# Performance work log

Measured on AMD Instinct MI355X. Metric: run time of the kernel, lower is better.

The kernel has to match this reference:

```python
import jax, jax.numpy as jnp
import numpy as np


def setup_inputs() -> dict:
    key = jax.random.key(0)
    k1, k2, k3, k4 = jax.random.split(key, 4)
    B, C = 32768, 10
    x = jax.random.normal(k1, (B, 1, 28, 28), dtype=jnp.float32)
    linear_weight = jax.random.normal(k2, (4 * 14 * 14 + 1 + 2, C), dtype=jnp.float32)
    linear_bias = jax.random.normal(k3, (C,), dtype=jnp.float32)
    sampler_weights = jax.random.normal(k4, (4,), dtype=jnp.float32)
    return {"x": x, "linear_weight": linear_weight, "linear_bias": linear_bias,
            "sampler_weights": sampler_weights}


def reference(x, linear_weight, linear_bias, sampler_weights):
    # Closed-form simulation of the 4-qubit circuits:
    # RY(t)|0> -> <Z>=cos(t); after CX(0,1): <Z1> = cos(t0)*cos(t1); CX(2,3) likewise.
    B = x.shape[0]
    # Extract non-overlapping 2x2 patches in row-major order -> (B, 196, 4)
    p = x[:, 0].reshape(B, 14, 2, 14, 2).transpose(0, 1, 3, 2, 4).reshape(B, 196, 4)
    c = jnp.cos(p)
    # quanvolution_circuit per patch: [cos a, cos a cos b, cos c, cos c cos d]
    feats = jnp.stack([c[..., 0], c[..., 0] * c[..., 1],
                       c[..., 2], c[..., 2] * c[..., 3]], axis=-1)  # (B,196,4)
    qfeat = feats.reshape(B, 784)
    # fully_connected_circuit on qfeat[:, :4]: mean of the four post-CX <Z>
    cf = jnp.cos(qfeat[:, :4])
    qfc = (cf[:, 0] + cf[:, 0] * cf[:, 1] + cf[:, 2] + cf[:, 2] * cf[:, 3]) / 4.0  # (B,)
    # sampler_circuit: sequential RY angles add on wires 0 and 1
    t0 = qfeat[:, 0] + sampler_weights[0] + sampler_weights[2]
    t1 = qfeat[:, 1] + sampler_weights[1] + sampler_weights[3]
    z0 = jnp.cos(t0)
    z1 = z0 * jnp.cos(t1)
    sampler = jax.nn.softmax(jnp.stack([z0, z1], axis=-1), axis=-1)  # (B,2)
    combined = jnp.concatenate([qfeat, qfc[:, None], sampler], axis=-1)  # (B,787)
    logits = combined @ linear_weight + linear_bias
    return jax.nn.log_softmax(logits, axis=-1)
```

## Files before the change

### kernel.cpp

```cpp
#include <hip/hip_runtime.h>


#define ROWF 128

__global__ __launch_bounds__(256, 2)
void qml_fused(const float* __restrict__ x,
               const float* __restrict__ wm,
               const float* __restrict__ bias,
               const float* __restrict__ sw,
               float* __restrict__ out,
               int B)
{
    __shared__ float lds[2][64 * ROWF];

    const int t = threadIdx.x;
    const int lane = t & 63;
    const int wv = __builtin_amdgcn_readfirstlane((int)(t >> 6));
    const int g = blockIdx.x;

    int sample = g * 64 + lane;
    const bool s_ok = (sample < B);
    if (sample >= B) sample = B - 1;

    const float* xb[7];
    int d0[7], d1[7];
#pragma unroll
    for (int k = 0; k < 7; ++k) {
        const int f = k * 256 + t;
        const int s = f / 28;
        const int c = f - 28 * s;
        int sg = g * 64 + s; if (sg >= B) sg = B - 1;
        xb[k] = x + (size_t)sg * 784 + 4 * c;
        const int m2 = (s & 15) << 1;
        d0[k] = s * ROWF + ((4 * c) ^ m2);
        d1[k] = s * ROWF + ((4 * c + 2) ^ m2);
    }

    const int i_loc = wv >> 1;
    const int jbase = 7 * (wv & 1);
    const int o_top = i_loc * 56 + 2 * jbase;
    const int m2c = (lane & 15) << 1;

    float acc[10];
#pragma unroll
    for (int c = 0; c < 10; ++c) acc[c] = 0.0f;
    float q0 = 0.f, q1 = 0.f, q2 = 0.f, q3 = 0.f;

    float4 pre[7];

#pragma unroll
    for (int k = 0; k < 7; ++k) pre[k] = *(const float4*)(xb[k]);
#pragma unroll
    for (int k = 0; k < 7; ++k) {
        *(float2*)(&lds[0][0] + d0[k]) = make_float2(pre[k].x, pre[k].y);
        *(float2*)(&lds[0][0] + d1[k]) = make_float2(pre[k].z, pre[k].w);
    }
    __syncthreads();

#pragma unroll
    for (int ps = 0; ps < 7; ++ps) {
        const int cur = ps & 1, nxt = cur ^ 1;

        if (ps < 6) {
#pragma unroll
            for (int k = 0; k < 7; ++k)
                pre[k] = *(const float4*)(xb[k] + (ps + 1) * 112);
        }

        const float* __restrict__ row = &lds[cur][0] + lane * ROWF;
        const int p0 = (2 * ps + i_loc) * 14 + jbase;

#pragma unroll
        for (int tt = 0; tt < 7; ++tt) {
            const int ot = o_top + 2 * tt;
            const float2 a = *(const float2*)(row + (ot ^ m2c));
            const float2 b = *(const float2*)(row + ((ot + 28) ^ m2c));

            const float c0 = __cosf(a.x);
            const float c1 = __cosf(a.y);
            const float c2 = __cosf(b.x);
            const float c3 = __cosf(b.y);
            const float v0 = c0, v1 = c0 * c1, v2 = c2, v3 = c2 * c3;

            if (ps == 0 && wv == 0 && tt == 0) { q0 = v0; q1 = v1; q2 = v2; q3 = v3; }

            const float* __restrict__ wr = wm + 40 * (p0 + tt);
#pragma unroll
            for (int c = 0; c < 10; ++c)
                acc[c] += v0 * wr[c] + v1 * wr[10 + c] + v2 * wr[20 + c] + v3 * wr[30 + c];
        }

        if (ps < 6) {
#pragma unroll
            for (int k = 0; k < 7; ++k) {
                *(float2*)(&lds[nxt][0] + d0[k]) = make_float2(pre[k].x, pre[k].y);
                *(float2*)(&lds[nxt][0] + d1[k]) = make_float2(pre[k].z, pre[k].w);
            }
        }
        __syncthreads();
    }

    float* __restrict__ red = &lds[0][0];
    if (wv != 0) {
#pragma unroll
        for (int c = 0; c < 10; ++c) red[(wv - 1) * 704 + lane * 11 + c] = acc[c];
    }
    __syncthreads();

    if (wv == 0) {
#pragma unroll
        for (int c = 0; c < 10; ++c)
            acc[c] += red[lane * 11 + c] + red[704 + lane * 11 + c]
                    + red[1408 + lane * 11 + c];

        const float f0 = __cosf(q0), f1 = __cosf(q1);
        const float f2 = __cosf(q2), f3 = __cosf(q3);
        const float qfc = (f0 + f0 * f1 + f2 + f2 * f3) * 0.25f;

        const float t0 = q0 + sw[0] + sw[2];
        const float t1 = q1 + sw[1] + sw[3];
        const float z0 = __cosf(t0);
        const float z1 = z0 * __cosf(t1);
        const float e0 = __expf(z0);
        const float e1 = __expf(z1);
        const float inv = 1.0f / (e0 + e1);
        const float s0 = e0 * inv, s1 = e1 * inv;

        const float* __restrict__ wt = wm + 7840;
#pragma unroll
        for (int c = 0; c < 10; ++c)
            acc[c] += qfc * wt[c] + s0 * wt[10 + c] + s1 * wt[20 + c] + bias[c];

        float m = acc[0];
#pragma unroll
        for (int c = 1; c < 10; ++c) m = fmaxf(m, acc[c]);
        float ssum = 0.0f;
#pragma unroll
        for (int c = 0; c < 10; ++c) ssum += __expf(acc[c] - m);
        const float lse = __logf(ssum) + m;

        if (s_ok) {
            float* __restrict__ orow = out + (size_t)sample * 10;
#pragma unroll
            for (int c = 0; c < 10; ++c) orow[c] = acc[c] - lse;
        }
    }
}

extern "C" void kernel_launch(void* const* d_in, const int* in_sizes, int n_in,
                              void* d_out, int out_size, void* d_ws, size_t ws_size,
                              hipStream_t stream) {
    const float* x    = (const float*)d_in[0];
    const float* w    = (const float*)d_in[1];
    const float* bias = (const float*)d_in[2];
    const float* sw   = (const float*)d_in[3];
    float* out = (float*)d_out;

    const int B = in_sizes[0] / 784;
    const int nblk = (B + 63) / 64;
    qml_fused<<<nblk, 256, 0, stream>>>(x, w, bias, sw, out, B);
}
```

Baseline: 173.1 us.

## Replace scalar FMA projection with bf16 MFMA using LDS-staged weights

```diff
diff --git a/kernel.cpp b/kernel.cpp
--- a/kernel.cpp
+++ b/kernel.cpp
@@ -1,117 +1,171 @@
 #include <hip/hip_runtime.h>
 
 
-#define ROWF 128
+typedef __attribute__((ext_vector_type(8))) short short8;
+typedef __attribute__((ext_vector_type(4))) float floatx4;
+
+__device__ __forceinline__ unsigned short f2bf(float f) {
+    unsigned u = __float_as_uint(f);
+    return (unsigned short)((u + 0x7FFFu + ((u >> 16) & 1u)) >> 16);
+}
+
+#define A_OFF  28672
+#define QF_OFF 61440
 
 __global__ __launch_bounds__(256, 2)
-void qml_fused(const float* __restrict__ x,
-               const float* __restrict__ wm,
-               const float* __restrict__ bias,
-               const float* __restrict__ sw,
-               float* __restrict__ out,
-               int B)
+void qml_mfma(const float* __restrict__ x,
+              const float* __restrict__ wm,
+              const float* __restrict__ bias,
+              const float* __restrict__ sw,
+              float* __restrict__ out,
+              int B)
 {
-    __shared__ float lds[2][64 * ROWF];
+    __shared__ __align__(16) char smem[62464];
+    float* rawW = (float*)(smem + A_OFF);
+    float* qf   = (float*)(smem + QF_OFF);
+    float* lg   = (float*)(smem + A_OFF);
 
     const int t = threadIdx.x;
     const int lane = t & 63;
     const int wv = __builtin_amdgcn_readfirstlane((int)(t >> 6));
     const int g = blockIdx.x;
 
-    int sample = g * 64 + lane;
-    const bool s_ok = (sample < B);
-    if (sample >= B) sample = B - 1;
-
-    const float* xb[7];
-    int d0[7], d1[7];
-#pragma unroll
-    for (int k = 0; k < 7; ++k) {
-        const int f = k * 256 + t;
-        const int s = f / 28;
-        const int c = f - 28 * s;
-        int sg = g * 64 + s; if (sg >= B) sg = B - 1;
-        xb[k] = x + (size_t)sg * 784 + 4 * c;
-        const int m2 = (s & 15) << 1;
-        d0[k] = s * ROWF + ((4 * c) ^ m2);
-        d1[k] = s * ROWF + ((4 * c + 2) ^ m2);
-    }
-
-    const int i_loc = wv >> 1;
-    const int jbase = 7 * (wv & 1);
-    const int o_top = i_loc * 56 + 2 * jbase;
-    const int m2c = (lane & 15) << 1;
-
-    float acc[10];
-#pragma unroll
-    for (int c = 0; c < 10; ++c) acc[c] = 0.0f;
-    float q0 = 0.f, q1 = 0.f, q2 = 0.f, q3 = 0.f;
-
-    float4 pre[7];
-
-#pragma unroll
-    for (int k = 0; k < 7; ++k) pre[k] = *(const float4*)(xb[k]);
-#pragma unroll
-    for (int k = 0; k < 7; ++k) {
-        *(float2*)(&lds[0][0] + d0[k]) = make_float2(pre[k].x, pre[k].y);
-        *(float2*)(&lds[0][0] + d1[k]) = make_float2(pre[k].z, pre[k].w);
-    }
-    __syncthreads();
-
-#pragma unroll
-    for (int ps = 0; ps < 7; ++ps) {
-        const int cur = ps & 1, nxt = cur ^ 1;
-
-        if (ps < 6) {
-#pragma unroll
-            for (int k = 0; k < 7; ++k)
-                pre[k] = *(const float4*)(xb[k] + (ps + 1) * 112);
-        }
-
-        const float* __restrict__ row = &lds[cur][0] + lane * ROWF;
-        const int p0 = (2 * ps + i_loc) * 14 + jbase;
-
-#pragma unroll
-        for (int tt = 0; tt < 7; ++tt) {
-            const int ot = o_top + 2 * tt;
-            const float2 a = *(const float2*)(row + (ot ^ m2c));
-            const float2 b = *(const float2*)(row + ((ot + 28) ^ m2c));
-
-            const float c0 = __cosf(a.x);
-            const float c1 = __cosf(a.y);
-            const float c2 = __cosf(b.x);
-            const float c3 = __cosf(b.y);
-            const float v0 = c0, v1 = c0 * c1, v2 = c2, v3 = c2 * c3;
-
-            if (ps == 0 && wv == 0 && tt == 0) { q0 = v0; q1 = v1; q2 = v2; q3 = v3; }
-
-            const float* __restrict__ wr = wm + 40 * (p0 + tt);
-#pragma unroll
-            for (int c = 0; c < 10; ++c)
-                acc[c] += v0 * wr[c] + v1 * wr[10 + c] + v2 * wr[20 + c] + v3 * wr[30 + c];
-        }
-
-        if (ps < 6) {
-#pragma unroll
-            for (int k = 0; k < 7; ++k) {
-                *(float2*)(&lds[nxt][0] + d0[k]) = make_float2(pre[k].x, pre[k].y);
-                *(float2*)(&lds[nxt][0] + d1[k]) = make_float2(pre[k].z, pre[k].w);
+    for (int i = t; i < 7870; i += 256) rawW[i] = wm[i];
+    __syncthreads();
+
+#pragma unroll
+    for (int c = 0; c < 7; ++c) {
+        const int CH = c * 256 + t;
+        const int T = CH >> 6, L = CH & 63;
+        const int n = L & 15, kq = L >> 4;
+        short8 v;
+#pragma unroll
+        for (int j = 0; j < 8; ++j) {
+            const int kh = 32 * T + kq * 8 + j;
+            const int sg = kh >> 7, kl = kh & 127;
+            float w = 0.0f;
+            if (kl < 112 && n < 10) w = rawW[(112 * sg + kl) * 10 + n];
+            v[j] = (short)f2bf(w);
+        }
+        *(short8*)(smem + CH * 16) = v;
+    }
+    __syncthreads();
+
+    int st_pr[4], st_s[4], st_unit[4];
+    const float* st_px[4];
+#pragma unroll
+    for (int c4 = 0; c4 < 4; ++c4) {
+        const int G = c4 * 256 + t;
+        const int s = G >> 4, pr = G & 15;
+        st_s[c4] = s; st_pr[c4] = pr;
+        st_unit[c4] = s * 16 + (pr ^ (s & 15));
+        int sglob = g * 64 + s; if (sglob >= B) sglob = B - 1;
+        const int r = (pr >= 7) ? 1 : 0;
+        const int cq = (pr >= 7) ? (pr - 7) : pr;
+        st_px[c4] = x + (size_t)sglob * 784 + r * 56 + 4 * cq;
+    }
+
+    floatx4 tp[4], bt[4];
+
+    const int sA = wv * 16 + (lane & 15);
+    const int swzA = sA & 15;
+    const int prq = lane >> 4;
+
+    floatx4 acc = {0.f, 0.f, 0.f, 0.f};
+
+#pragma unroll
+    for (int c4 = 0; c4 < 4; ++c4)
+        if (st_pr[c4] < 14) {
+            tp[c4] = *(const floatx4*)(st_px[c4]);
+            bt[c4] = *(const floatx4*)(st_px[c4] + 28);
+        }
+#pragma unroll
+    for (int c4 = 0; c4 < 4; ++c4) {
+        float f0 = 0.f, f1 = 0.f, f2 = 0.f, f3 = 0.f;
+        float f4 = 0.f, f5 = 0.f, f6 = 0.f, f7 = 0.f;
+        if (st_pr[c4] < 14) {
+            const float c0 = __cosf(tp[c4].x), c1 = __cosf(tp[c4].y);
+            const float c2 = __cosf(bt[c4].x), c3 = __cosf(bt[c4].y);
+            f0 = c0; f1 = c0 * c1; f2 = c2; f3 = c2 * c3;
+            const float c4_ = __cosf(tp[c4].z), c5 = __cosf(tp[c4].w);
+            const float c6 = __cosf(bt[c4].z), c7 = __cosf(bt[c4].w);
+            f4 = c4_; f5 = c4_ * c5; f6 = c6; f7 = c6 * c7;
+            if (st_pr[c4] == 0) {
+                float* qd = qf + st_s[c4] * 4;
+                qd[0] = f0; qd[1] = f1; qd[2] = f2; qd[3] = f3;
             }
         }
+        short8 v;
+        v[0] = (short)f2bf(f0); v[1] = (short)f2bf(f1);
+        v[2] = (short)f2bf(f2); v[3] = (short)f2bf(f3);
+        v[4] = (short)f2bf(f4); v[5] = (short)f2bf(f5);
+        v[6] = (short)f2bf(f6); v[7] = (short)f2bf(f7);
+        *(short8*)(smem + A_OFF + st_unit[c4] * 16) = v;
+    }
+    __syncthreads();
+
+#pragma unroll
+    for (int sg = 0; sg < 7; ++sg) {
+        const int buf = sg & 1;
+
+        if (sg < 6) {
+#pragma unroll
+            for (int c4 = 0; c4 < 4; ++c4)
+                if (st_pr[c4] < 14) {
+                    tp[c4] = *(const floatx4*)(st_px[c4] + (sg + 1) * 112);
+                    bt[c4] = *(const floatx4*)(st_px[c4] + (sg + 1) * 112 + 28);
+                }
+        }
+
+#pragma unroll
+        for (int tl = 0; tl < 4; ++tl) {
+            const int pr = 4 * tl + prq;
+            const short8 a = *(const short8*)(smem + A_OFF + buf * 16384
+                                              + (sA * 16 + (pr ^ swzA)) * 16);
+            const short8 b = *(const short8*)(smem + ((4 * sg + tl) * 64 + lane) * 16);
+            acc = __builtin_amdgcn_mfma_f32_16x16x32_bf16(a, b, acc, 0, 0, 0);
+        }
+
+        if (sg < 6) {
+#pragma unroll
+            for (int c4 = 0; c4 < 4; ++c4) {
+                float f0 = 0.f, f1 = 0.f, f2 = 0.f, f3 = 0.f;
+                float f4 = 0.f, f5 = 0.f, f6 = 0.f, f7 = 0.f;
+                if (st_pr[c4] < 14) {
+                    const float c0 = __cosf(tp[c4].x), c1 = __cosf(tp[c4].y);
+                    const float c2 = __cosf(bt[c4].x), c3 = __cosf(bt[c4].y);
+                    f0 = c0; f1 = c0 * c1; f2 = c2; f3 = c2 * c3;
+                    const float c4_ = __cosf(tp[c4].z), c5 = __cosf(tp[c4].w);
+                    const float c6 = __cosf(bt[c4].z), c7 = __cosf(bt[c4].w);
+                    f4 = c4_; f5 = c4_ * c5; f6 = c6; f7 = c6 * c7;
+                }
+                short8 v;
+                v[0] = (short)f2bf(f0); v[1] = (short)f2bf(f1);
+                v[2] = (short)f2bf(f2); v[3] = (short)f2bf(f3);
+                v[4] = (short)f2bf(f4); v[5] = (short)f2bf(f5);
+                v[6] = (short)f2bf(f6); v[7] = (short)f2bf(f7);
+                *(short8*)(smem + A_OFF + (buf ^ 1) * 16384 + st_unit[c4] * 16) = v;
+            }
+        }
         __syncthreads();
     }
 
-    float* __restrict__ red = &lds[0][0];
-    if (wv != 0) {
-#pragma unroll
-        for (int c = 0; c < 10; ++c) red[(wv - 1) * 704 + lane * 11 + c] = acc[c];
-    }
-    __syncthreads();
-
-    if (wv == 0) {
-#pragma unroll
-        for (int c = 0; c < 10; ++c)
-            acc[c] += red[lane * 11 + c] + red[704 + lane * 11 + c]
-                    + red[1408 + lane * 11 + c];
+    {
+        const int n = lane & 15;
+        const int rbase = wv * 16 + (lane >> 4) * 4;
+        if (n < 10) {
+#pragma unroll
+            for (int r = 0; r < 4; ++r) lg[(rbase + r) * 11 + n] = acc[r];
+        }
+    }
+    __syncthreads();
+
+#pragma unroll
+    for (int e = t; e < 640; e += 256) {
+        const int s2 = e / 10, c2 = e - 10 * s2;
+        float logit = lg[s2 * 11 + c2];
+        const float q0 = qf[s2 * 4 + 0], q1 = qf[s2 * 4 + 1];
+        const float q2 = qf[s2 * 4 + 2], q3 = qf[s2 * 4 + 3];
 
         const float f0 = __cosf(q0), f1 = __cosf(q1);
         const float f2 = __cosf(q2), f3 = __cosf(q3);
@@ -121,29 +175,28 @@
         const float t1 = q1 + sw[1] + sw[3];
         const float z0 = __cosf(t0);
         const float z1 = z0 * __cosf(t1);
-        const float e0 = __expf(z0);
-        const float e1 = __expf(z1);
+        const float e0 = __expf(z0), e1 = __expf(z1);
         const float inv = 1.0f / (e0 + e1);
-        const float s0 = e0 * inv, s1 = e1 * inv;
 
         const float* __restrict__ wt = wm + 7840;
-#pragma unroll
-        for (int c = 0; c < 10; ++c)
-            acc[c] += qfc * wt[c] + s0 * wt[10 + c] + s1 * wt[20 + c] + bias[c];
-
-        float m = acc[0];
-#pragma unroll
-        for (int c = 1; c < 10; ++c) m = fmaxf(m, acc[c]);
-        float ssum = 0.0f;
-#pragma unroll
-        for (int c = 0; c < 10; ++c) ssum += __expf(acc[c] - m);
-        const float lse = __logf(ssum) + m;
-
-        if (s_ok) {
-            float* __restrict__ orow = out + (size_t)sample * 10;
-#pragma unroll
-            for (int c = 0; c < 10; ++c) orow[c] = acc[c] - lse;
-        }
+        logit += bias[c2] + qfc * wt[c2] + (e0 * inv) * wt[10 + c2]
+                          + (e1 * inv) * wt[20 + c2];
+        lg[s2 * 11 + c2] = logit;
+    }
+    __syncthreads();
+
+#pragma unroll
+    for (int e = t; e < 640; e += 256) {
+        const int s2 = e / 10, c2 = e - 10 * s2;
+        float m = -3.4e38f;
+#pragma unroll
+        for (int k = 0; k < 10; ++k) m = fmaxf(m, lg[s2 * 11 + k]);
+        float ss = 0.0f;
+#pragma unroll
+        for (int k = 0; k < 10; ++k) ss += __expf(lg[s2 * 11 + k] - m);
+        const float lse = __logf(ss) + m;
+        if (g * 64 + s2 < B)
+            out[(size_t)g * 640 + e] = lg[s2 * 11 + c2] - lse;
     }
 }
 
@@ -158,5 +211,5 @@
 
     const int B = in_sizes[0] / 784;
     const int nblk = (B + 63) / 64;
-    qml_fused<<<nblk, 256, 0, stream>>>(x, w, bias, sw, out, B);
+    qml_mfma<<<nblk, 256, 0, stream>>>(x, w, bias, sw, out, B);
 }
```

New measurement: 162.2 us. -6.3%, faster.
